# Kernel optimization log

Measured on AMD Instinct MI355X. Metric: run time of the kernel, lower is better.

Reference implementation:

```python
import jax, jax.numpy as jnp
import numpy as np


def setup_inputs() -> dict:
    key = jax.random.key(0)
    ks = jax.random.split(key, 6)
    B, H, F, X, T = 8, 32, 8, 128, 256
    z0 = jax.random.normal(ks[0], (B, H, X), jnp.float32)
    xi = jax.random.normal(ks[1], (B, F, X, T), jnp.float32)
    A = jax.random.normal(ks[2], (H, H), jnp.float32) * 0.1
    Gw = jax.random.normal(ks[3], (H, F, H), jnp.float32) * 0.1
    Wr = jax.random.normal(ks[4], (X, H, H, H), jnp.float32) * 1e-4
    Wi = jax.random.normal(ks[5], (X, H, H, H), jnp.float32) * 1e-4
    return {"z0": z0, "xi": xi, "A": A, "Gw": Gw, "Wr": Wr, "Wi": Wi}


def reference(z0, xi, A, Gw, Wr, Wi):
    # z0: (B, H, X); xi: (B, F, X, T)
    B, Hc, X = z0.shape
    T = xi.shape[-1]

    # Initial guess u(t) = z0 for all t (reconstruction of the fixed-point seed).
    u = jnp.broadcast_to(z0[..., None], (B, Hc, X, T))

    # Linear SPDE right-hand side: Fu = A u, Gu = Gw u.
    Fu = jnp.einsum('ih,bhxt->bixt', A, u)
    Gu = jnp.einsum('ifh,bhxt->bifxt', Gw, u)          # (B, H, F, X, T)
    Guxi = jnpum = None
    Guxi = jnp.einsum('bifxt,bfxt->bixt', Gu, xi)
    Hu = Fu + Guxi                                      # (B, H, X, T)

    # Spatial FFT (axis 2) + fftshift, as in the torch module.
    H_ft = jnp.fft.fftshift(jnp.fft.fft(Hu, axis=2), axes=2)    # complex64
    z0_ft = jnp.fft.fftshift(jnp.fft.fft(z0, axis=2), axes=2)   # (B, H, X)

    # Per-Fourier-mode complex-linear CDE vector field weights.
    W = (Wr + 1j * Wi).astype(jnp.complex64)            # (X, H, H, H)

    # Control path X(t): (B, X, T, H); Euler increments at the knots.
    Hp = jnp.transpose(H_ft, (0, 2, 3, 1))
    dX = Hp[:, :, 1:, :] - Hp[:, :, :-1, :]             # (B, X, T-1, H)
    z_init = jnp.transpose(z0_ft, (0, 2, 1))            # (B, X, H)

    def step(z, dx):
        # f(z)[b, x, i, c] = sum_j W[x, i, c, j] z[b, x, j]
        fz = jnp.einsum('xicj,bxj->bxic', W, z)
        z_new = z + jnp.einsum('bxic,bxc->bxi', fz, dx)  # dz = f(z) . dX
        return z_new, z_new

    _, zs = jax.lax.scan(step, z_init, jnp.moveaxis(dX, 2, 0))
    zs = jnp.concatenate([z_init[None], zs], axis=0)    # (T, B, X, H)
    z_all = jnp.transpose(zs, (1, 3, 2, 0))             # (B, H, X, T)

    u_new = jnp.fft.ifft(jnp.fft.ifftshift(z_all, axes=2), axis=2)
    return u_new.real
```

## Files before the change

### kernel.cpp

```cpp
#include <hip/hip_runtime.h>
#include <math.h>

#define Bc 8
#define Hc 32
#define Fc 8
#define Xc 128
#define Tc 256

typedef __bf16 bf16x8 __attribute__((ext_vector_type(8)));
typedef float f32x4 __attribute__((ext_vector_type(4)));

__device__ __forceinline__ int bitrev7(int x) { return (int)(__brev((unsigned)x) >> 25); }

__device__ __forceinline__ unsigned pack_bf16(float a, float b) {
    unsigned ua = __float_as_uint(a);
    unsigned ub = __float_as_uint(b);
    ua = (ua + 0x7FFFu + ((ua >> 16) & 1u)) >> 16;
    ub = (ub + 0x7FFFu + ((ub >> 16) & 1u)) & 0xFFFF0000u;
    return (ua & 0xFFFFu) | ub;
}
__device__ __forceinline__ float bf16_val(float a) {
    unsigned ua = __float_as_uint(a);
    ua = (ua + 0x7FFFu + ((ua >> 16) & 1u)) & 0xFFFF0000u;
    return __uint_as_float(ua);
}

__device__ __forceinline__ void fft32x128(float2* buf, float sign) {
    __shared__ float2 tw[128];
    int tid = threadIdx.x;
    if (tid >= 1 && tid < 128) {
        int h = 1 << (31 - __builtin_clz((unsigned)tid));
        int pos = tid - h;
        float sn, cs;
        __sincosf(3.14159265358979f * (float)pos / (float)h, &sn, &cs);
        tw[tid] = make_float2(cs, sn);
    }
    for (int half = 1; half < 128; half <<= 1) {
        __syncthreads();
        for (int g = threadIdx.x; g < 32 * 64; g += 256) {
            int row = g >> 6, j = g & 63;
            int pos = j & (half - 1);
            int i0 = ((j & ~(half - 1)) << 1) + pos;
            float2* p = buf + row * 128;
            float2 a = p[i0];
            float2 bb = p[i0 + half];
            float2 twv = tw[half + pos];
            float cs = twv.x, sn = sign * twv.y;
            float2 bw = make_float2(cs * bb.x - sn * bb.y, cs * bb.y + sn * bb.x);
            p[i0] = make_float2(a.x + bw.x, a.y + bw.y);
            p[i0 + half] = make_float2(a.x - bw.x, a.y - bw.y);
        }
    }
    __syncthreads();
}

__global__ void k_pre(const float* __restrict__ z0, const float* __restrict__ A,
                      const float* __restrict__ Gw, float* __restrict__ Fz,
                      float* __restrict__ Gz, float2* __restrict__ Z0ft) {
    __shared__ float z0l[Hc * Xc];
    __shared__ float2 cbuf[Hc * Xc];
    int b = blockIdx.x;
    int tid = threadIdx.x;
    for (int idx = tid; idx < Hc * Xc; idx += 256) z0l[idx] = z0[b * Hc * Xc + idx];
    __syncthreads();
    for (int idx = tid; idx < Hc * Xc; idx += 256) {
        int i = idx >> 7, x = idx & 127;
        float s = 0.f;
        for (int h = 0; h < Hc; ++h) s += A[i * Hc + h] * z0l[h * 128 + x];
        Fz[b * Hc * Xc + idx] = s;
    }
    for (int idx = tid; idx < Hc * Fc * Xc; idx += 256) {
        int i = idx >> 10, f = (idx >> 7) & 7, x = idx & 127;
        float s = 0.f;
        for (int h = 0; h < Hc; ++h) s += Gw[(i * Fc + f) * Hc + h] * z0l[h * 128 + x];
        Gz[b * Hc * Fc * Xc + idx] = s;
    }
    for (int idx = tid; idx < Hc * Xc; idx += 256) {
        int h = idx >> 7, x = idx & 127;
        cbuf[h * 128 + bitrev7(x)] = make_float2(z0l[h * 128 + x], 0.f);
    }
    fft32x128(cbuf, -1.f);
    for (int idx = tid; idx < Xc * Hc; idx += 256) {
        int xs = idx >> 5, h = idx & 31;
        Z0ft[(b * Xc + xs) * Hc + h] = cbuf[h * 128 + ((xs + 64) & 127)];
    }
}

__global__ void k_spec(const float* __restrict__ xi, const float* __restrict__ Fz,
                       const float* __restrict__ Gz, float2* __restrict__ Hft) {
    __shared__ float xil[Fc * Xc];
    __shared__ float2 cbuf[Hc * Xc];
    int bid = blockIdx.x;
    int b = bid >> 8, t = bid & 255;
    int tid = threadIdx.x;
    for (int idx = tid; idx < Fc * Xc; idx += 256) {
        int f = idx >> 7, x = idx & 127;
        xil[idx] = xi[((b * Fc + f) * Xc + x) * Tc + t];
    }
    __syncthreads();
    for (int idx = tid; idx < Hc * Xc; idx += 256) {
        int i = idx >> 7, x = idx & 127;
        float hu = Fz[b * Hc * Xc + idx];
        const float* gzp = Gz + (b * Hc + i) * (Fc * Xc) + x;
#pragma unroll
        for (int f = 0; f < Fc; ++f) hu += gzp[f * 128] * xil[f * 128 + x];
        cbuf[i * 128 + bitrev7(x)] = make_float2(hu, 0.f);
    }
    fft32x128(cbuf, -1.f);
    for (int idx = tid; idx < Xc * Hc; idx += 256) {
        int xs = idx >> 5, i = idx & 31;
        Hft[((long)(b * Xc + xs) * Tc + t) * Hc + i] = cbuf[i * 128 + ((xs + 64) & 127)];
    }
}

#define ML_DW 16448
#define B_DW  1152
#define SCAN_LDS 150016

__device__ __forceinline__ void build_B(unsigned* Bb, int w, int tt, int c,
                                        float2 hp, float2 hn, float sc) {
    float dre = (hn.x - hp.x) * sc;
    float dim = (hn.y - hp.y) * sc;
    float hre = bf16_val(dre), hmim = bf16_val(-dim), him = bf16_val(dim);
    int n0 = w * 4 + tt * 2;
    Bb[n0 * 36 + c] = pack_bf16(hre, hmim);
    Bb[(n0 + 1) * 36 + c] = pack_bf16(him, hre);
    Bb[576 + n0 * 36 + c] = pack_bf16(dre - hre, (-dim) - hmim);
    Bb[576 + (n0 + 1) * 36 + c] = pack_bf16(dim - him, dre - hre);
}

__global__ __launch_bounds__(512, 2) void k_scan(const float* __restrict__ Wr,
                                                 const float* __restrict__ Wi,
                                                 const float2* __restrict__ Hft,
                                                 const float2* __restrict__ Z0ft,
                                                 float2* __restrict__ Zall) {
    extern __shared__ unsigned char smem[];
    float* Mlf = (float*)smem;
    unsigned* Aw = (unsigned*)smem;
    unsigned* Bd = (unsigned*)(smem + 131584);
    float* zlf = (float*)(smem + 140800);
    float2* zstc = (float2*)(smem + 141824);

    int tid = threadIdx.x;
    int x = blockIdx.x >> 1, g = blockIdx.x & 1;
    int lane = tid & 63, wid = tid >> 6;
    int isProd = (wid < 4);
    int w = wid & 3;
    int b = g * 4 + w;

    const float* wrp = Wr + (size_t)x * 32768;
    const float* wip = Wi + (size_t)x * 32768;
    for (int idx = tid; idx < 32768; idx += 512) {
        int j = idx & 31, cc = (idx >> 5) & 31, ii = idx >> 10;
        int r = ii * 32 + j;
        int pd = r * 32 + (((cc >> 2) ^ (r & 7)) << 2) + (cc & 3);
        Aw[pd] = pack_bf16(wrp[(ii * 32 + cc) * 32 + j], wip[(ii * 32 + cc) * 32 + j]);
    }
    __syncthreads();

    size_t bx = (size_t)(b * Xc + x);
    const float2* Hrow = Hft + bx * (Tc * Hc);
    float2* Zrow = Zall + bx * (Hc * Tc);
    int jq = lane >> 5, il = lane & 31;

    uint4 af[16][2];
    float2 Hp2 = make_float2(0.f, 0.f), Hn2 = make_float2(0.f, 0.f);
    float2 zr = make_float2(0.f, 0.f);

    if (isProd) {
        int n16 = lane & 15, q = lane >> 4;
        int rbase = w * 256 + n16;
#pragma unroll
        for (int mt = 0; mt < 16; ++mt) {
            int r = rbase + mt * 16;
#pragma unroll
            for (int kf = 0; kf < 2; ++kf) {
                int cg = (kf * 4 + q) ^ (r & 7);
                af[mt][kf] = *(const uint4*)(Aw + r * 32 + cg * 4);
            }
        }
        float2 ha = Hrow[jq * 32 + il];
        float2 hb = Hrow[(1 + jq) * 32 + il];
        build_B(Bd, w, jq, il, ha, hb, 1.f);
        Hp2 = Hrow[(2 + jq) * 32 + il];
        Hn2 = Hrow[(3 + jq) * 32 + il];
    } else {
        zr = Z0ft[bx * Hc + il];
        if (jq == 0) {
            ((float2*)(zlf + w * 64))[il] = zr;
            zstc[w * 256 + il] = zr;
        }
    }
    __syncthreads();

#pragma unroll 1
    for (int k = 0; k <= 128; ++k) {
        if (isProd) {
            if (k < 128) {
                int bk = k & 1;
                {
                    int n = lane & 15, q = lane >> 4;
                    const unsigned* Bb = Bd + bk * B_DW;
                    bf16x8 bh0 = __builtin_bit_cast(bf16x8, *(const uint4*)(Bb + n * 36 + q * 4));
                    bf16x8 bh1 = __builtin_bit_cast(bf16x8, *(const uint4*)(Bb + n * 36 + 16 + q * 4));
                    bf16x8 bl0 = __builtin_bit_cast(bf16x8, *(const uint4*)(Bb + 576 + n * 36 + q * 4));
                    bf16x8 bl1 = __builtin_bit_cast(bf16x8, *(const uint4*)(Bb + 576 + n * 36 + 16 + q * 4));
                    float* Mb = Mlf + bk * ML_DW;
#pragma unroll
                    for (int mt = 0; mt < 16; ++mt) {
                        f32x4 acc = {0.f, 0.f, 0.f, 0.f};
                        acc = __builtin_amdgcn_mfma_f32_16x16x32_bf16(
                            __builtin_bit_cast(bf16x8, af[mt][0]), bh0, acc, 0, 0, 0);
                        acc = __builtin_amdgcn_mfma_f32_16x16x32_bf16(
                            __builtin_bit_cast(bf16x8, af[mt][1]), bh1, acc, 0, 0, 0);
                        acc = __builtin_amdgcn_mfma_f32_16x16x32_bf16(
                            __builtin_bit_cast(bf16x8, af[mt][0]), bl0, acc, 0, 0, 0);
                        acc = __builtin_amdgcn_mfma_f32_16x16x32_bf16(
                            __builtin_bit_cast(bf16x8, af[mt][1]), bl1, acc, 0, 0, 0);
                        int i = w * 8 + (mt >> 1);
                        int jgp = (((mt & 1) * 4) + q) ^ ((mt >> 1) & 7);
                        *(f32x4*)(Mb + n * 1028 + i * 32 + jgp * 4) = acc;
                    }
                }
                if (k < 127) {
                    float sc = (2 * (k + 1) + 1 + jq <= 255) ? 1.f : 0.f;
                    build_B(Bd + ((k + 1) & 1) * B_DW, w, jq, il, Hp2, Hn2, sc);
                }
                if (k < 126) {
                    int kc = k + 2;
                    Hp2 = Hrow[(2 * kc + jq) * 32 + il];
                    int t2 = 2 * kc + 1 + jq;
                    if (t2 > 255) t2 = 255;
                    Hn2 = Hrow[t2 * 32 + il];
                }
            }
        } else if (k > 0) {
            int kc = k - 1;
            int bk = kc & 1;
#pragma unroll
            for (int s = 0; s < 2; ++s) {
                int t = 2 * kc + 1 + s;
                if (t > 255) break;
                const float* base = Mlf + bk * ML_DW + (w * 4 + s * 2) * 1028 + il * 32;
                float4 mr[4], mi[4];
#pragma unroll
                for (int gg = 0; gg < 4; ++gg) {
                    int jg = (((jq * 4 + gg) ^ (il & 7)) << 2);
                    mr[gg] = *(const float4*)(base + jg);
                    mi[gg] = *(const float4*)(base + 1028 + jg);
                }
                const float4* zf4 = (const float4*)(zlf + w * 64);
                float yR = 0.f, yI = 0.f;
#pragma unroll
                for (int gg = 0; gg < 4; ++gg) {
                    float4 za = zf4[jq * 8 + gg * 2];
                    float4 zb = zf4[jq * 8 + gg * 2 + 1];
                    yR += mr[gg].x * za.x - mi[gg].x * za.y + mr[gg].y * za.z - mi[gg].y * za.w
                        + mr[gg].z * zb.x - mi[gg].z * zb.y + mr[gg].w * zb.z - mi[gg].w * zb.w;
                    yI += mr[gg].x * za.y + mi[gg].x * za.x + mr[gg].y * za.w + mi[gg].y * za.z
                        + mr[gg].z * zb.y + mi[gg].z * zb.x + mr[gg].w * zb.w + mi[gg].w * zb.z;
                }
                yR += __shfl_xor(yR, 32);
                yI += __shfl_xor(yI, 32);
                zr.x += yR;
                zr.y += yI;
                if (jq == 0) {
                    ((float2*)(zlf + w * 64))[il] = zr;
                    zstc[w * 256 + (t & 7) * 32 + il] = zr;
                }
                if ((t & 7) == 7) {
                    int t0 = t - 7;
                    int i2 = lane >> 1, tb = (lane & 1) * 4;
                    float2 v0 = zstc[w * 256 + (tb + 0) * 32 + i2];
                    float2 v1 = zstc[w * 256 + (tb + 1) * 32 + i2];
                    float2 v2 = zstc[w * 256 + (tb + 2) * 32 + i2];
                    float2 v3 = zstc[w * 256 + (tb + 3) * 32 + i2];
                    *(float4*)(Zrow + i2 * Tc + t0 + tb) = make_float4(v0.x, v0.y, v1.x, v1.y);
                    *(float4*)(Zrow + i2 * Tc + t0 + tb + 2) = make_float4(v2.x, v2.y, v3.x, v3.y);
                }
            }
        }
        __syncthreads();
    }
}

__global__ void k_post(const float2* __restrict__ Zall, float* __restrict__ out) {
    __shared__ float2 cbuf[32 * 128];
    int bid = blockIdx.x;
    int b = bid >> 8, i = (bid >> 3) & 31, tq = bid & 7;
    int t0 = tq * 32;
    int tid = threadIdx.x;
    for (int idx = tid; idx < 128 * 32; idx += 256) {
        int k = idx >> 5, tc = idx & 31;
        int xg = (k + 64) & 127;
        cbuf[tc * 128 + bitrev7(k)] =
            Zall[((long)(b * Xc + xg) * Hc + i) * Tc + t0 + tc];
    }
    fft32x128(cbuf, +1.f);
    const float inv = 1.0f / 128.0f;
    for (int idx = tid; idx < 128 * 32; idx += 256) {
        int xs = idx >> 5, tc = idx & 31;
        out[((long)(b * Hc + i) * Xc + xs) * Tc + t0 + tc] = cbuf[tc * 128 + xs].x * inv;
    }
}

extern "C" void kernel_launch(void* const* d_in, const int* in_sizes, int n_in,
                              void* d_out, int out_size, void* d_ws, size_t ws_size,
                              hipStream_t stream) {
    const float* z0 = (const float*)d_in[0];
    const float* xi = (const float*)d_in[1];
    const float* A = (const float*)d_in[2];
    const float* Gw = (const float*)d_in[3];
    const float* Wr = (const float*)d_in[4];
    const float* Wi = (const float*)d_in[5];
    float* out = (float*)d_out;
    char* ws = (char*)d_ws;

    float2* Hft = (float2*)(ws);
    float2* Zall = (float2*)(ws + 67108864);
    float2* Z0ft = (float2*)(ws + 134217728);
    float* Fz = (float*)(ws + 134479872);
    float* Gz = (float*)(ws + 134610944);

    (void)hipFuncSetAttribute((const void*)k_scan,
                              hipFuncAttributeMaxDynamicSharedMemorySize, SCAN_LDS);

    k_pre<<<Bc, 256, 0, stream>>>(z0, A, Gw, Fz, Gz, Z0ft);
    k_spec<<<Bc * Tc, 256, 0, stream>>>(xi, Fz, Gz, Hft);
    k_scan<<<Xc * 2, 512, SCAN_LDS, stream>>>(Wr, Wi, Hft, Z0ft, Zall);
    k_post<<<Bc * Hc * 8, 256, 0, stream>>>(Zall, out);
}
```

Before: 478.7 us.

## Transpose xi for coalesced loads and split scan MFMA work across eight producer waves

New measurement: 596.9 us. 1.25x slower.

```diff
diff --git a/kernel.cpp b/kernel.cpp
--- a/kernel.cpp
+++ b/kernel.cpp
@@ -54,6 +54,27 @@
     __syncthreads();
 }
 
+__global__ void k_xit(const float* __restrict__ xi, float* __restrict__ xiT) {
+    __shared__ float tile[32][33];
+    int bid = blockIdx.x;
+    int bf = bid >> 3, tt = bid & 7;
+    int t0 = tt * 32;
+    int tid = threadIdx.x;
+    for (int xt = 0; xt < 4; ++xt) {
+        int x0 = xt * 32;
+        __syncthreads();
+        for (int idx = tid; idx < 1024; idx += 256) {
+            int xr = idx >> 5, tc = idx & 31;
+            tile[xr][tc] = xi[((size_t)bf * Xc + x0 + xr) * Tc + t0 + tc];
+        }
+        __syncthreads();
+        for (int idx = tid; idx < 1024; idx += 256) {
+            int tr = idx >> 5, xc = idx & 31;
+            xiT[((size_t)bf * Tc + t0 + tr) * Xc + x0 + xc] = tile[xc][tr];
+        }
+    }
+}
+
 __global__ void k_pre(const float* __restrict__ z0, const float* __restrict__ A,
                       const float* __restrict__ Gw, float* __restrict__ Fz,
                       float* __restrict__ Gz, float2* __restrict__ Z0ft) {
@@ -86,7 +107,7 @@
     }
 }
 
-__global__ void k_spec(const float* __restrict__ xi, const float* __restrict__ Fz,
+__global__ void k_spec(const float* __restrict__ xiT, const float* __restrict__ Fz,
                        const float* __restrict__ Gz, float2* __restrict__ Hft) {
     __shared__ float xil[Fc * Xc];
     __shared__ float2 cbuf[Hc * Xc];
@@ -95,7 +116,7 @@
     int tid = threadIdx.x;
     for (int idx = tid; idx < Fc * Xc; idx += 256) {
         int f = idx >> 7, x = idx & 127;
-        xil[idx] = xi[((b * Fc + f) * Xc + x) * Tc + t];
+        xil[idx] = xiT[((size_t)(b * Fc + f) * Tc + t) * Xc + x];
     }
     __syncthreads();
     for (int idx = tid; idx < Hc * Xc; idx += 256) {
@@ -129,7 +150,7 @@
     Bb[576 + (n0 + 1) * 36 + c] = pack_bf16(dim - him, dre - hre);
 }
 
-__global__ __launch_bounds__(512, 2) void k_scan(const float* __restrict__ Wr,
+__global__ __launch_bounds__(768, 3) void k_scan(const float* __restrict__ Wr,
                                                  const float* __restrict__ Wi,
                                                  const float2* __restrict__ Hft,
                                                  const float2* __restrict__ Z0ft,
@@ -144,13 +165,14 @@
     int tid = threadIdx.x;
     int x = blockIdx.x >> 1, g = blockIdx.x & 1;
     int lane = tid & 63, wid = tid >> 6;
-    int isProd = (wid < 4);
-    int w = wid & 3;
+    int isProd = (wid < 8);
+    int p = wid;
+    int w = isProd ? (wid & 3) : (wid - 8);
     int b = g * 4 + w;
 
     const float* wrp = Wr + (size_t)x * 32768;
     const float* wip = Wi + (size_t)x * 32768;
-    for (int idx = tid; idx < 32768; idx += 512) {
+    for (int idx = tid; idx < 32768; idx += 768) {
         int j = idx & 31, cc = (idx >> 5) & 31, ii = idx >> 10;
         int r = ii * 32 + j;
         int pd = r * 32 + (((cc >> 2) ^ (r & 7)) << 2) + (cc & 3);
@@ -163,15 +185,15 @@
     float2* Zrow = Zall + bx * (Hc * Tc);
     int jq = lane >> 5, il = lane & 31;
 
-    uint4 af[16][2];
+    uint4 af[8][2];
     float2 Hp2 = make_float2(0.f, 0.f), Hn2 = make_float2(0.f, 0.f);
     float2 zr = make_float2(0.f, 0.f);
 
     if (isProd) {
         int n16 = lane & 15, q = lane >> 4;
-        int rbase = w * 256 + n16;
-#pragma unroll
-        for (int mt = 0; mt < 16; ++mt) {
+        int rbase = p * 128 + n16;
+#pragma unroll
+        for (int mt = 0; mt < 8; ++mt) {
             int r = rbase + mt * 16;
 #pragma unroll
             for (int kf = 0; kf < 2; ++kf) {
@@ -179,11 +201,13 @@
                 af[mt][kf] = *(const uint4*)(Aw + r * 32 + cg * 4);
             }
         }
-        float2 ha = Hrow[jq * 32 + il];
-        float2 hb = Hrow[(1 + jq) * 32 + il];
-        build_B(Bd, w, jq, il, ha, hb, 1.f);
-        Hp2 = Hrow[(2 + jq) * 32 + il];
-        Hn2 = Hrow[(3 + jq) * 32 + il];
+        if (p < 4) {
+            float2 ha = Hrow[jq * 32 + il];
+            float2 hb = Hrow[(1 + jq) * 32 + il];
+            build_B(Bd, w, jq, il, ha, hb, 1.f);
+            Hp2 = Hrow[(2 + jq) * 32 + il];
+            Hn2 = Hrow[(3 + jq) * 32 + il];
+        }
     } else {
         zr = Z0ft[bx * Hc + il];
         if (jq == 0) {
@@ -207,7 +231,7 @@
                     bf16x8 bl1 = __builtin_bit_cast(bf16x8, *(const uint4*)(Bb + 576 + n * 36 + 16 + q * 4));
                     float* Mb = Mlf + bk * ML_DW;
 #pragma unroll
-                    for (int mt = 0; mt < 16; ++mt) {
+                    for (int mt = 0; mt < 8; ++mt) {
                         f32x4 acc = {0.f, 0.f, 0.f, 0.f};
                         acc = __builtin_amdgcn_mfma_f32_16x16x32_bf16(
                             __builtin_bit_cast(bf16x8, af[mt][0]), bh0, acc, 0, 0, 0);
@@ -217,48 +241,56 @@
                             __builtin_bit_cast(bf16x8, af[mt][0]), bl0, acc, 0, 0, 0);
                         acc = __builtin_amdgcn_mfma_f32_16x16x32_bf16(
                             __builtin_bit_cast(bf16x8, af[mt][1]), bl1, acc, 0, 0, 0);
-                        int i = w * 8 + (mt >> 1);
-                        int jgp = (((mt & 1) * 4) + q) ^ ((mt >> 1) & 7);
+                        int i = p * 4 + (mt >> 1);
+                        int jgp = (((mt & 1) * 4) + q) ^ (i & 7);
                         *(f32x4*)(Mb + n * 1028 + i * 32 + jgp * 4) = acc;
                     }
                 }
-                if (k < 127) {
-                    float sc = (2 * (k + 1) + 1 + jq <= 255) ? 1.f : 0.f;
-                    build_B(Bd + ((k + 1) & 1) * B_DW, w, jq, il, Hp2, Hn2, sc);
-                }
-                if (k < 126) {
-                    int kc = k + 2;
-                    Hp2 = Hrow[(2 * kc + jq) * 32 + il];
-                    int t2 = 2 * kc + 1 + jq;
-                    if (t2 > 255) t2 = 255;
-                    Hn2 = Hrow[t2 * 32 + il];
+                if (p < 4) {
+                    if (k < 127) {
+                        float sc = (2 * (k + 1) + 1 + jq <= 255) ? 1.f : 0.f;
+                        build_B(Bd + ((k + 1) & 1) * B_DW, w, jq, il, Hp2, Hn2, sc);
+                    }
+                    if (k < 126) {
+                        int kc = k + 2;
+                        Hp2 = Hrow[(2 * kc + jq) * 32 + il];
+                        int t2 = 2 * kc + 1 + jq;
+                        if (t2 > 255) t2 = 255;
+                        Hn2 = Hrow[t2 * 32 + il];
+                    }
                 }
             }
         } else if (k > 0) {
             int kc = k - 1;
             int bk = kc & 1;
+            float4 mr[2][4], mi[2][4];
+#pragma unroll
+            for (int s = 0; s < 2; ++s) {
+                int t = 2 * kc + 1 + s;
+                if (t <= 255) {
+                    const float* base = Mlf + bk * ML_DW + (w * 4 + s * 2) * 1028 + il * 32;
+#pragma unroll
+                    for (int gg = 0; gg < 4; ++gg) {
+                        int jg = (((jq * 4 + gg) ^ (il & 7)) << 2);
+                        mr[s][gg] = *(const float4*)(base + jg);
+                        mi[s][gg] = *(const float4*)(base + 1028 + jg);
+                    }
+                }
+            }
 #pragma unroll
             for (int s = 0; s < 2; ++s) {
                 int t = 2 * kc + 1 + s;
                 if (t > 255) break;
-                const float* base = Mlf + bk * ML_DW + (w * 4 + s * 2) * 1028 + il * 32;
-                float4 mr[4], mi[4];
-#pragma unroll
-                for (int gg = 0; gg < 4; ++gg) {
-                    int jg = (((jq * 4 + gg) ^ (il & 7)) << 2);
-                    mr[gg] = *(const float4*)(base + jg);
-                    mi[gg] = *(const float4*)(base + 1028 + jg);
-                }
                 const float4* zf4 = (const float4*)(zlf + w * 64);
                 float yR = 0.f, yI = 0.f;
 #pragma unroll
                 for (int gg = 0; gg < 4; ++gg) {
                     float4 za = zf4[jq * 8 + gg * 2];
                     float4 zb = zf4[jq * 8 + gg * 2 + 1];
-                    yR += mr[gg].x * za.x - mi[gg].x * za.y + mr[gg].y * za.z - mi[gg].y * za.w
-                        + mr[gg].z * zb.x - mi[gg].z * zb.y + mr[gg].w * zb.z - mi[gg].w * zb.w;
-                    yI += mr[gg].x * za.y + mi[gg].x * za.x + mr[gg].y * za.w + mi[gg].y * za.z
-                        + mr[gg].z * zb.y + mi[gg].z * zb.x + mr[gg].w * zb.w + mi[gg].w * zb.z;
+                    yR += mr[s][gg].x * za.x - mi[s][gg].x * za.y + mr[s][gg].y * za.z - mi[s][gg].y * za.w
+                        + mr[s][gg].z * zb.x - mi[s][gg].z * zb.y + mr[s][gg].w * zb.z - mi[s][gg].w * zb.w;
+                    yI += mr[s][gg].x * za.y + mi[s][gg].x * za.x + mr[s][gg].y * za.w + mi[s][gg].y * za.z
+                        + mr[s][gg].z * zb.y + mi[s][gg].z * zb.x + mr[s][gg].w * zb.w + mi[s][gg].w * zb.z;
                 }
                 yR += __shfl_xor(yR, 32);
                 yI += __shfl_xor(yI, 32);
@@ -321,12 +353,14 @@
     float2* Z0ft = (float2*)(ws + 134217728);
     float* Fz = (float*)(ws + 134479872);
     float* Gz = (float*)(ws + 134610944);
+    float* xiT = (float*)(ws + 67108864);
 
     (void)hipFuncSetAttribute((const void*)k_scan,
                               hipFuncAttributeMaxDynamicSharedMemorySize, SCAN_LDS);
 
+    k_xit<<<Bc * Fc * 8, 256, 0, stream>>>(xi, xiT);
     k_pre<<<Bc, 256, 0, stream>>>(z0, A, Gw, Fz, Gz, Z0ft);
-    k_spec<<<Bc * Tc, 256, 0, stream>>>(xi, Fz, Gz, Hft);
-    k_scan<<<Xc * 2, 512, SCAN_LDS, stream>>>(Wr, Wi, Hft, Z0ft, Zall);
+    k_spec<<<Bc * Tc, 256, 0, stream>>>(xiT, Fz, Gz, Hft);
+    k_scan<<<Xc * 2, 768, SCAN_LDS, stream>>>(Wr, Wi, Hft, Z0ft, Zall);
     k_post<<<Bc * Hc * 8, 256, 0, stream>>>(Zall, out);
 }
```
